# Kernel optimization log

Measured on AMD Instinct MI355X. Metric: run time of the kernel, lower is better.

The kernel has to match this reference:

```python
import jax, jax.numpy as jnp
import numpy as np
import math

VOCAB, D, H, NL, L, B = 50257, 768, 12, 4, 1024, 2
DH = D // H
DFF = 4 * D
ALPHA = 0.25
NEG = -1e9


def _ln(x, g, b, eps=1e-5):
    mu = x.mean(-1, keepdims=True)
    var = ((x - mu) ** 2).mean(-1, keepdims=True)
    return (x - mu) * jax.lax.rsqrt(var + eps) * g + b


def setup_inputs() -> dict:
    key = jax.random.key(0)
    ks = jax.random.split(key, 16)
    s = 0.02
    tokens = jax.random.randint(ks[0], (B, L), 0, VOCAB)
    timelike_mask = jax.random.randint(ks[1], (NL, D), 0, 2).astype(jnp.int32)
    embed = jax.random.normal(ks[2], (VOCAB, D), jnp.float32) * s
    pos_emb = jax.random.normal(ks[3], (L, D), jnp.float32) * s
    wq = jax.random.normal(ks[4], (NL, D, D), jnp.float32) * s
    wk = jax.random.normal(ks[5], (NL, D, D), jnp.float32) * s
    wv = jax.random.normal(ks[6], (NL, D, D), jnp.float32) * s
    wo = jax.random.normal(ks[7], (NL, D, D), jnp.float32) * s
    ff_w1 = jax.random.normal(ks[8], (NL, DFF, D), jnp.float32) * s
    ff_b1 = jnp.zeros((NL, DFF), jnp.float32)
    ff_w2 = jax.random.normal(ks[9], (NL, D, DFF), jnp.float32) * s
    ff_b2 = jnp.zeros((NL, D), jnp.float32)
    ln1_g = jnp.ones((NL, D), jnp.float32); ln1_b = jnp.zeros((NL, D), jnp.float32)
    ln2_g = jnp.ones((NL, D), jnp.float32); ln2_b = jnp.zeros((NL, D), jnp.float32)
    lnf_g = jnp.ones((D,), jnp.float32); lnf_b = jnp.zeros((D,), jnp.float32)
    return dict(tokens=tokens, timelike_mask=timelike_mask, embed=embed, pos_emb=pos_emb,
                wq=wq, wk=wk, wv=wv, wo=wo,
                ln1_g=ln1_g, ln1_b=ln1_b, ln2_g=ln2_g, ln2_b=ln2_b,
                ff_w1=ff_w1, ff_b1=ff_b1, ff_w2=ff_w2, ff_b2=ff_b2,
                lnf_g=lnf_g, lnf_b=lnf_b)


def reference(tokens, timelike_mask, embed, pos_emb, wq, wk, wv, wo,
              ln1_g, ln1_b, ln2_g, ln2_b, ff_w1, ff_b1, ff_w2, ff_b2,
              lnf_g, lnf_b):
    Bc, Lc = tokens.shape
    scale = math.sqrt(DH)
    # embeddings: token + learned position
    h = embed[tokens] + pos_emb[None, :Lc]  # (B,L,D)
    # additive causal mask, matching torch's -inf attention_mask convention
    causal = jnp.where(jnp.tril(jnp.ones((Lc, Lc), bool)), 0.0, NEG)[None, None]  # (1,1,L,L)
    for i in range(NL):
        xn = _ln(h, ln1_g[i], ln1_b[i])
        # nn.Linear(bias=False): y = x @ W.T, W is (out,in)
        q = jnp.einsum('bld,od->blo', xn, wq[i]).reshape(Bc, Lc, H, DH).astype(jnp.float32)
        k = jnp.einsum('bld,od->blo', xn, wk[i]).reshape(Bc, Lc, H, DH).astype(jnp.float32)
        v = jnp.einsum('bld,od->blo', xn, wv[i]).reshape(Bc, Lc, H, DH)
        # Minkowski term: scores_std - 2*alpha*(Q*P_t)K^T  ==  (Q*(1-2*alpha*m)) K^T
        m = timelike_mask[i].astype(jnp.float32).reshape(H, DH)  # per-head timelike directions
        q_eff = q * (1.0 - 2.0 * ALPHA * m)[None, None]
        scores = jnp.einsum('bqhd,bkhd->bhqk', q_eff, k) / scale + causal
        aw = jax.nn.softmax(scores, axis=-1)  # dropout=0 (eval)
        attn = jnp.einsum('bhqk,bkhd->bqhd', aw, v).reshape(Bc, Lc, D)
        h = h + jnp.einsum('bld,od->blo', attn, wo[i])
        xn2 = _ln(h, ln2_g[i], ln2_b[i])
        ff = jax.nn.gelu(jnp.einsum('bld,fd->blf', xn2, ff_w1[i]) + ff_b1[i], approximate=False)
        h = h + jnp.einsum('blf,df->bld', ff, ff_w2[i]) + ff_b2[i]
    h = _ln(h, lnf_g, lnf_b)
    logits = jnp.einsum('bld,vd->blv', h, embed)  # tied LM head
    return logits
```

## Files before the change

kernel.cpp:

```cpp
#include <hip/hip_runtime.h>
#include <math.h>

#define VOCABSZ 50257
#define VPAD 50304
#define DMODEL 768
#define NHEAD 12
#define NLAYER 4
#define SEQ 1024
#define BATCH 2
#define DHEAD 64
#define DFFN 3072
#define BT (BATCH * SEQ)
#define NBH (BATCH * NHEAD)

typedef __attribute__((ext_vector_type(8))) short bf16x8;
typedef __attribute__((ext_vector_type(4))) float f32x4;

__device__ __forceinline__ ushort f2bf(float f) {
  uint u = __builtin_bit_cast(uint, f);
  u = (u + 0x7fffu + ((u >> 16) & 1u)) >> 16;
  return (ushort)u;
}

__device__ __forceinline__ void gl_lds16(const ushort* g, ushort* l) {
  __builtin_amdgcn_global_load_lds(
      (const __attribute__((address_space(1))) void*)g,
      (__attribute__((address_space(3))) void*)l, 16, 0, 0);
}

__global__ __launch_bounds__(256) void conv4_kernel(
    const float* __restrict__ src, ushort* __restrict__ dst, int n4) {
  int i = blockIdx.x * 256 + threadIdx.x;
  if (i >= n4) return;
  float4 v = reinterpret_cast<const float4*>(src)[i];
  reinterpret_cast<ushort4*>(dst)[i] =
      make_ushort4(f2bf(v.x), f2bf(v.y), f2bf(v.z), f2bf(v.w));
}

__global__ __launch_bounds__(256) void conv_qkv_kernel(
    const float* __restrict__ src, ushort* __restrict__ dst, int qoff4) {
  const int per4 = DMODEL * DMODEL / 4;
  int i = blockIdx.x * 256 + threadIdx.x;
  if (i >= NLAYER * per4) return;
  int layer = i / per4, rem = i % per4;
  float4 v = reinterpret_cast<const float4*>(src)[i];
  reinterpret_cast<ushort4*>(dst)[(size_t)layer * (3 * per4) + qoff4 + rem] =
      make_ushort4(f2bf(v.x), f2bf(v.y), f2bf(v.z), f2bf(v.w));
}

__global__ __launch_bounds__(256) void conv_embed_kernel(
    const float* __restrict__ emb, ushort* __restrict__ dst) {
  int i = blockIdx.x * 256 + threadIdx.x;
  if (i >= VPAD * DMODEL / 4) return;
  int row = (i * 4) / DMODEL;
  ushort4 o = make_ushort4(0, 0, 0, 0);
  if (row < VOCABSZ) {
    float4 v = reinterpret_cast<const float4*>(emb)[i];
    o = make_ushort4(f2bf(v.x), f2bf(v.y), f2bf(v.z), f2bf(v.w));
  }
  reinterpret_cast<ushort4*>(dst)[i] = o;
}

__global__ __launch_bounds__(256) void embed_kernel(
    const int* __restrict__ tok, const float* __restrict__ emb,
    const float* __restrict__ pos, float* __restrict__ h) {
  int row = blockIdx.x;
  int l = row % SEQ;
  int t = tok[row];
  int tid = threadIdx.x;
#pragma unroll
  for (int j = 0; j < 3; ++j) {
    int c = tid + j * 256;
    h[(size_t)row * DMODEL + c] =
        emb[(size_t)t * DMODEL + c] + pos[(size_t)l * DMODEL + c];
  }
}

template <int KS, bool RBIAS>
__global__ __launch_bounds__(256) void ln_kernel(
    float* __restrict__ h, const float* __restrict__ part,
    const float* __restrict__ rb, const float* __restrict__ g,
    const float* __restrict__ bta, ushort* __restrict__ o) {
  __shared__ float red[8];
  int row = blockIdx.x;
  int tid = threadIdx.x;
  float* xr = h + (size_t)row * DMODEL;
  float v[3];
  float s = 0.f, sq = 0.f;
#pragma unroll
  for (int j = 0; j < 3; ++j) {
    int c = tid + j * 256;
    float a = xr[c];
    if (RBIAS) a += rb[c];
    if (KS > 0) {
#pragma unroll
      for (int z = 0; z < KS; ++z)
        a += part[(size_t)z * BT * DMODEL + (size_t)row * DMODEL + c];
      xr[c] = a;
    }
    v[j] = a;
    s += a;
    sq += a * a;
  }
#pragma unroll
  for (int off = 1; off < 64; off <<= 1) {
    s += __shfl_xor(s, off);
    sq += __shfl_xor(sq, off);
  }
  int wid = tid >> 6;
  if ((tid & 63) == 0) { red[wid * 2] = s; red[wid * 2 + 1] = sq; }
  __syncthreads();
  float S = red[0] + red[2] + red[4] + red[6];
  float SQ = red[1] + red[3] + red[5] + red[7];
  float mu = S * (1.0f / DMODEL);
  float var = SQ * (1.0f / DMODEL) - mu * mu;
  float r = rsqrtf(var + 1e-5f);
  ushort* orow = o + (size_t)row * DMODEL;
#pragma unroll
  for (int j = 0; j < 3; ++j) {
    int c = tid + j * 256;
    orow[c] = f2bf((v[j] - mu) * r * g[c] + bta[c]);
  }
}

__global__ __launch_bounds__(256) void vtrans_kernel(
    const ushort* __restrict__ v, ushort* __restrict__ vt) {
  __shared__ ushort t[64][65];
  int z = blockIdx.y, b = z / NHEAD, hh = z % NHEAD;
  int key0 = blockIdx.x * 64;
  int tid = threadIdx.x;
#pragma unroll
  for (int p = 0; p < 16; ++p) {
    int idx = tid + p * 256;
    int kk = idx >> 6, d = idx & 63;
    t[kk][d] = v[((size_t)(b * SEQ + key0 + kk)) * DMODEL + hh * DHEAD + d];
  }
  __syncthreads();
#pragma unroll
  for (int p = 0; p < 16; ++p) {
    int idx = tid + p * 256;
    int d = idx >> 6, kk = idx & 63;
    vt[((size_t)(z * 64 + d)) * SEQ + key0 + kk] = t[kk][d];
  }
}

__global__ __launch_bounds__(256) void fattn_kernel(
    const ushort* __restrict__ q, const ushort* __restrict__ k,
    const ushort* __restrict__ vt, ushort* __restrict__ o) {
  __shared__ __align__(16) ushort Ks[64 * 64];
  __shared__ __align__(16) ushort Vs[64 * 64];
  __shared__ __align__(16) ushort Ps[4][16][80];
  const int z = blockIdx.y, b = z / NHEAD, hh = z % NHEAD;
  const int q0 = (gridDim.x - 1 - blockIdx.x) * 64;
  const int tid = threadIdx.x, w = tid >> 6, l = tid & 63;
  const int fr = l & 15, ks = l >> 4;
  const int qrow = q0 + w * 16 + fr;
  const ushort* qp = q + (size_t)(b * SEQ + qrow) * DMODEL + hh * DHEAD;
  const bf16x8 qf0 = *reinterpret_cast<const bf16x8*>(qp + ks * 8);
  const bf16x8 qf1 = *reinterpret_cast<const bf16x8*>(qp + 32 + ks * 8);

  const int srow = w * 16 + (l >> 3);
  const int sslot = l & 7;

  f32x4 acc_o[4] = {};
  float mrun = -1e30f, lrun = 0.f;

  for (int k0 = 0; k0 <= q0; k0 += 64) {
#pragma unroll
    for (int c = 0; c < 2; ++c) {
      int r = srow + c * 8;
      int g = sslot ^ (r & 7);
      gl_lds16(k + (size_t)(b * SEQ + k0 + r) * DMODEL + hh * DHEAD + g * 8,
               Ks + (w * 16 + c * 8) * 64);
      gl_lds16(vt + (size_t)(z * 64 + r) * SEQ + k0 + g * 8,
               Vs + (w * 16 + c * 8) * 64);
    }
    __syncthreads();
    f32x4 acc_s[4] = {};
#pragma unroll
    for (int kstep = 0; kstep < 2; ++kstep) {
      const bf16x8 qf = kstep ? qf1 : qf0;
#pragma unroll
      for (int kb = 0; kb < 4; ++kb) {
        int ra = kb * 16 + fr;
        bf16x8 af = *reinterpret_cast<const bf16x8*>(
            Ks + ra * 64 + (((kstep * 4 + ks) ^ (ra & 7)) * 8));
        acc_s[kb] =
            __builtin_amdgcn_mfma_f32_16x16x32_bf16(af, qf, acc_s[kb], 0, 0, 0);
      }
    }
    const bool diag = (k0 == q0);
    float pm = -1e30f;
    float sv[4][4];
#pragma unroll
    for (int kb = 0; kb < 4; ++kb)
#pragma unroll
      for (int r = 0; r < 4; ++r) {
        float s = acc_s[kb][r];
        if (diag && (k0 + kb * 16 + ks * 4 + r > qrow)) s = -1e30f;
        sv[kb][r] = s;
        pm = fmaxf(pm, s);
      }
    pm = fmaxf(pm, __shfl_xor(pm, 16));
    pm = fmaxf(pm, __shfl_xor(pm, 32));
    float mnew = fmaxf(mrun, pm);
    float scale = __expf(mrun - mnew);
    float psum = 0.f;
#pragma unroll
    for (int kb = 0; kb < 4; ++kb) {
      float p0 = __expf(sv[kb][0] - mnew);
      float p1 = __expf(sv[kb][1] - mnew);
      float p2 = __expf(sv[kb][2] - mnew);
      float p3 = __expf(sv[kb][3] - mnew);
      psum += (p0 + p1) + (p2 + p3);
      *reinterpret_cast<ushort4*>(&Ps[w][fr][kb * 16 + ks * 4]) =
          make_ushort4(f2bf(p0), f2bf(p1), f2bf(p2), f2bf(p3));
    }
    psum += __shfl_xor(psum, 16);
    psum += __shfl_xor(psum, 32);
    lrun = lrun * scale + psum;
    mrun = mnew;
#pragma unroll
    for (int db = 0; db < 4; ++db) acc_o[db] *= scale;
#pragma unroll
    for (int kstep = 0; kstep < 2; ++kstep) {
      bf16x8 pf =
          *reinterpret_cast<const bf16x8*>(&Ps[w][fr][kstep * 32 + ks * 8]);
#pragma unroll
      for (int db = 0; db < 4; ++db) {
        int rd = db * 16 + fr;
        bf16x8 vf = *reinterpret_cast<const bf16x8*>(
            Vs + rd * 64 + (((kstep * 4 + ks) ^ (rd & 7)) * 8));
        acc_o[db] =
            __builtin_amdgcn_mfma_f32_16x16x32_bf16(vf, pf, acc_o[db], 0, 0, 0);
      }
    }
    __syncthreads();
  }
  float rinv = 1.0f / lrun;
#pragma unroll
  for (int db = 0; db < 4; ++db) {
    ushort4 o4 =
        make_ushort4(f2bf(acc_o[db][0] * rinv), f2bf(acc_o[db][1] * rinv),
                     f2bf(acc_o[db][2] * rinv), f2bf(acc_o[db][3] * rinv));
    *reinterpret_cast<ushort4*>(o + (size_t)(b * SEQ + qrow) * DMODEL +
                                hh * DHEAD + db * 16 + ks * 4) = o4;
  }
}

template <bool QKV, bool BIAS, bool GELU, bool RES, bool OUTBF, bool SWZ,
          bool PART>
__global__ __launch_bounds__(256) void gemm_bf16_nt(
    const ushort* __restrict__ A, const ushort* __restrict__ B,
    const float* __restrict__ bias, const int* __restrict__ tmask,
    const float* __restrict__ res, float* __restrict__ Cf,
    ushort* __restrict__ Cb, int ldc, ushort* __restrict__ qb,
    ushort* __restrict__ kb, ushort* __restrict__ vb, int M, int K, int Nreal,
    int kchunk) {
  __shared__ __align__(16) ushort As[2][128 * 32];
  __shared__ __align__(16) ushort Bs[2][128 * 32];
  int bnx, bmy;
  if (SWZ) {
    int bid = blockIdx.x;
    int chunk = gridDim.x >> 3;
    int wgid = (bid & 7) * chunk + (bid >> 3);
    int mb = M >> 7;
    bmy = wgid % mb;
    bnx = wgid / mb;
  } else {
    bnx = blockIdx.x;
    bmy = blockIdx.y;
  }
  const int m0 = bmy * 128, n0 = bnx * 128;
  const int kbeg = PART ? blockIdx.z * kchunk : 0;
  const int kend = PART ? kbeg + kchunk : K;
  if (PART) Cf += (size_t)blockIdx.z * M * ldc;
  const int tid = threadIdx.x;
  const int w = tid >> 6, l = tid & 63;
  const int wr = w >> 1, wc = w & 1;
  const int fr = l & 15, ks = l >> 4;

  const int seg0 = w * 2, seg1 = w * 2 + 1;
  const int srow0 = seg0 * 16 + (l >> 2);
  const int srow1 = seg1 * 16 + (l >> 2);
  const int koff0 = (((l & 3) ^ ((srow0 >> 1) & 3))) * 8;
  const int koff1 = (((l & 3) ^ ((srow1 >> 1) & 3))) * 8;
  const ushort* A0 = A + (size_t)(m0 + srow0) * K + koff0;
  const ushort* A1 = A + (size_t)(m0 + srow1) * K + koff1;
  const ushort* B0 = B + (size_t)(n0 + srow0) * K + koff0;
  const ushort* B1 = B + (size_t)(n0 + srow1) * K + koff1;

  int aoff[4], boff[4];
#pragma unroll
  for (int i = 0; i < 4; ++i) {
    int ra = wr * 64 + i * 16 + fr;
    aoff[i] = ra * 32 + ((ks ^ ((ra >> 1) & 3)) * 8);
    int rb = wc * 64 + i * 16 + fr;
    boff[i] = rb * 32 + ((ks ^ ((rb >> 1) & 3)) * 8);
  }

  gl_lds16(A0 + kbeg, &As[0][seg0 * 512]);
  gl_lds16(A1 + kbeg, &As[0][seg1 * 512]);
  gl_lds16(B0 + kbeg, &Bs[0][seg0 * 512]);
  gl_lds16(B1 + kbeg, &Bs[0][seg1 * 512]);
  __syncthreads();

  f32x4 acc[4][4] = {};
  int cur = 0;
  for (int k0 = kbeg; k0 < kend; k0 += 32) {
    const int nxt = k0 + 32;
    if (nxt < kend) {
      gl_lds16(A0 + nxt, &As[cur ^ 1][seg0 * 512]);
      gl_lds16(A1 + nxt, &As[cur ^ 1][seg1 * 512]);
      gl_lds16(B0 + nxt, &Bs[cur ^ 1][seg0 * 512]);
      gl_lds16(B1 + nxt, &Bs[cur ^ 1][seg1 * 512]);
    }
    bf16x8 af[4], bfr[4];
#pragma unroll
    for (int i = 0; i < 4; ++i)
      af[i] = *reinterpret_cast<const bf16x8*>(&As[cur][aoff[i]]);
#pragma unroll
    for (int i = 0; i < 4; ++i)
      bfr[i] = *reinterpret_cast<const bf16x8*>(&Bs[cur][boff[i]]);
#pragma unroll
    for (int mi = 0; mi < 4; ++mi)
#pragma unroll
      for (int nj = 0; nj < 4; ++nj)
        acc[mi][nj] = __builtin_amdgcn_mfma_f32_16x16x32_bf16(
            af[mi], bfr[nj], acc[mi][nj], 0, 0, 0);
    __syncthreads();
    cur ^= 1;
  }

#pragma unroll
  for (int mi = 0; mi < 4; ++mi) {
#pragma unroll
    for (int nj = 0; nj < 4; ++nj) {
      int n = n0 + wc * 64 + nj * 16 + fr;
      if (n < Nreal) {
#pragma unroll
        for (int r = 0; r < 4; ++r) {
          int m = m0 + wr * 64 + mi * 16 + ks * 4 + r;
          float v = acc[mi][nj][r];
          if (PART) {
            Cf[(size_t)m * ldc + n] = v;
          } else if (QKV) {
            if (n < DMODEL) {
              v *= (1.0f - 0.5f * (float)tmask[n]) * 0.125f;
              qb[(size_t)m * DMODEL + n] = f2bf(v);
            } else if (n < 2 * DMODEL) {
              kb[(size_t)m * DMODEL + (n - DMODEL)] = f2bf(v);
            } else {
              vb[(size_t)m * DMODEL + (n - 2 * DMODEL)] = f2bf(v);
            }
          } else {
            if (BIAS) v += bias[n];
            if (GELU) v = 0.5f * v * (1.0f + erff(v * 0.70710678118f));
            if (RES) v += res[(size_t)m * ldc + n];
            if (OUTBF)
              Cb[(size_t)m * ldc + n] = f2bf(v);
            else
              Cf[(size_t)m * ldc + n] = v;
          }
        }
      }
    }
  }
}

extern "C" void kernel_launch(void* const* d_in, const int* in_sizes, int n_in,
                              void* d_out, int out_size, void* d_ws,
                              size_t ws_size, hipStream_t stream) {
  const int* tokens = (const int*)d_in[0];
  const int* tmask = (const int*)d_in[1];
  const float* embed = (const float*)d_in[2];
  const float* pos = (const float*)d_in[3];
  const float* wq = (const float*)d_in[4];
  const float* wk = (const float*)d_in[5];
  const float* wv = (const float*)d_in[6];
  const float* wo = (const float*)d_in[7];
  const float* ln1g = (const float*)d_in[8];
  const float* ln1b = (const float*)d_in[9];
  const float* ln2g = (const float*)d_in[10];
  const float* ln2b = (const float*)d_in[11];
  const float* fw1 = (const float*)d_in[12];
  const float* fb1 = (const float*)d_in[13];
  const float* fw2 = (const float*)d_in[14];
  const float* fb2 = (const float*)d_in[15];
  const float* lnfg = (const float*)d_in[16];
  const float* lnfb = (const float*)d_in[17];

  char* wp = (char*)d_ws;
  auto alloc = [&](size_t bytes) {
    void* p = wp;
    wp += (bytes + 255) & ~(size_t)255;
    return p;
  };
  float* h = (float*)alloc((size_t)BT * DMODEL * 4);
  float* part = (float*)alloc((size_t)4 * BT * DMODEL * 4);
  ushort* qb = (ushort*)alloc((size_t)BT * DMODEL * 2);
  ushort* kb = (ushort*)alloc((size_t)BT * DMODEL * 2);
  ushort* vb = (ushort*)alloc((size_t)BT * DMODEL * 2);
  ushort* vt = (ushort*)alloc((size_t)NBH * DHEAD * SEQ * 2);
  ushort* xn = (ushort*)alloc((size_t)BT * DMODEL * 2);
  ushort* ab = (ushort*)alloc((size_t)BT * DMODEL * 2);
  ushort* ffb = (ushort*)alloc((size_t)BT * DFFN * 2);
  ushort* wqkv_b = (ushort*)alloc((size_t)NLAYER * 3 * DMODEL * DMODEL * 2);
  ushort* wo_b = (ushort*)alloc((size_t)NLAYER * DMODEL * DMODEL * 2);
  ushort* fw1_b = (ushort*)alloc((size_t)NLAYER * DFFN * DMODEL * 2);
  ushort* fw2_b = (ushort*)alloc((size_t)NLAYER * DMODEL * DFFN * 2);
  ushort* emb_b = (ushort*)alloc((size_t)VPAD * DMODEL * 2);

  const int per4 = DMODEL * DMODEL / 4;
  conv_qkv_kernel<<<(NLAYER * per4 + 255) / 256, 256, 0, stream>>>(wq, wqkv_b, 0);
  conv_qkv_kernel<<<(NLAYER * per4 + 255) / 256, 256, 0, stream>>>(wk, wqkv_b, per4);
  conv_qkv_kernel<<<(NLAYER * per4 + 255) / 256, 256, 0, stream>>>(wv, wqkv_b, 2 * per4);
  conv4_kernel<<<(NLAYER * per4 + 255) / 256, 256, 0, stream>>>(wo, wo_b, NLAYER * per4);
  const int nff4 = NLAYER * DFFN * DMODEL / 4;
  conv4_kernel<<<(nff4 + 255) / 256, 256, 0, stream>>>(fw1, fw1_b, nff4);
  conv4_kernel<<<(nff4 + 255) / 256, 256, 0, stream>>>(fw2, fw2_b, nff4);
  conv_embed_kernel<<<(VPAD * DMODEL / 4 + 255) / 256, 256, 0, stream>>>(embed, emb_b);

  embed_kernel<<<BT, 256, 0, stream>>>(tokens, embed, pos, h);

  const dim3 gqkv(3 * DMODEL / 128, BT / 128);
  const dim3 gff(DFFN / 128, BT / 128);
  const dim3 gwo(DMODEL / 128, BT / 128, 2);
  const dim3 gff2(DMODEL / 128, BT / 128, 4);
  const dim3 gv((BT / 128) * (VPAD / 128));

  for (int i = 0; i < NLAYER; ++i) {
    if (i == 0)
      ln_kernel<0, false><<<BT, 256, 0, stream>>>(
          h, nullptr, nullptr, ln1g + i * DMODEL, ln1b + i * DMODEL, xn);
    else
      ln_kernel<4, true><<<BT, 256, 0, stream>>>(
          h, part, fb2 + (i - 1) * DMODEL, ln1g + i * DMODEL,
          ln1b + i * DMODEL, xn);

    gemm_bf16_nt<true, false, false, false, false, false, false>
        <<<gqkv, 256, 0, stream>>>(
            xn, wqkv_b + (size_t)i * 3 * DMODEL * DMODEL, nullptr,
            tmask + i * DMODEL, nullptr, nullptr, nullptr, 0, qb, kb, vb, BT,
            DMODEL, 3 * DMODEL, DMODEL);

    vtrans_kernel<<<dim3(SEQ / 64, NBH), 256, 0, stream>>>(vb, vt);

    fattn_kernel<<<dim3(SEQ / 64, NBH), 256, 0, stream>>>(qb, kb, vt, ab);

    gemm_bf16_nt<false, false, false, false, false, false, true>
        <<<gwo, 256, 0, stream>>>(
            ab, wo_b + (size_t)i * DMODEL * DMODEL, nullptr, nullptr, nullptr,
            part, nullptr, DMODEL, nullptr, nullptr, nullptr, BT, DMODEL,
            DMODEL, DMODEL / 2);

    ln_kernel<2, false><<<BT, 256, 0, stream>>>(
        h, part, nullptr, ln2g + i * DMODEL, ln2b + i * DMODEL, xn);

    gemm_bf16_nt<false, true, true, false, true, false, false>
        <<<gff, 256, 0, stream>>>(
            xn, fw1_b + (size_t)i * DFFN * DMODEL, fb1 + i * DFFN, nullptr,
            nullptr, nullptr, ffb, DFFN, nullptr, nullptr, nullptr, BT, DMODEL,
            DFFN, DMODEL);

    gemm_bf16_nt<false, false, false, false, false, false, true>
        <<<gff2, 256, 0, stream>>>(
            ffb, fw2_b + (size_t)i * DMODEL * DFFN, nullptr, nullptr, nullptr,
            part, nullptr, DMODEL, nullptr, nullptr, nullptr, BT, DFFN, DMODEL,
            DFFN / 4);
  }

  ln_kernel<4, true><<<BT, 256, 0, stream>>>(
      h, part, fb2 + (NLAYER - 1) * DMODEL, lnfg, lnfb, xn);

  gemm_bf16_nt<false, false, false, false, false, true, false>
      <<<gv, 256, 0, stream>>>(
          xn, emb_b, nullptr, nullptr, nullptr, (float*)d_out, nullptr,
          VOCABSZ, nullptr, nullptr, nullptr, BT, DMODEL, VOCABSZ, DMODEL);
}
```

Before: 973.1 us.

## Add 256x256 pipelined LM-head GEMM and fuse V transpose into QKV epilogue

Replaces the generic 128x128 LM-head GEMM with a dedicated 512-thread kernel using 256x256 tiles, a 4-stage LDS ring with three tiles prefetched, split MFMA phases with s_setprio, and an XCD-aware block swizzle. VPAD grows to a multiple of 256 so the tile grid covers it. The QKV GEMM epilogue now writes V directly in the transposed per-head layout, removing the separate vtrans kernel and the intermediate V buffer. Risks include higher register and LDS pressure in the new kernel, extra padded work, and strided ushort4 stores for the transposed V.

```diff
diff --git a/kernel.cpp b/kernel.cpp
--- a/kernel.cpp
+++ b/kernel.cpp
@@ -2,7 +2,7 @@
 #include <math.h>
 
 #define VOCABSZ 50257
-#define VPAD 50304
+#define VPAD 50432
 #define DMODEL 768
 #define NHEAD 12
 #define NLAYER 4
@@ -120,27 +120,6 @@
   for (int j = 0; j < 3; ++j) {
     int c = tid + j * 256;
     orow[c] = f2bf((v[j] - mu) * r * g[c] + bta[c]);
-  }
-}
-
-__global__ __launch_bounds__(256) void vtrans_kernel(
-    const ushort* __restrict__ v, ushort* __restrict__ vt) {
-  __shared__ ushort t[64][65];
-  int z = blockIdx.y, b = z / NHEAD, hh = z % NHEAD;
-  int key0 = blockIdx.x * 64;
-  int tid = threadIdx.x;
-#pragma unroll
-  for (int p = 0; p < 16; ++p) {
-    int idx = tid + p * 256;
-    int kk = idx >> 6, d = idx & 63;
-    t[kk][d] = v[((size_t)(b * SEQ + key0 + kk)) * DMODEL + hh * DHEAD + d];
-  }
-  __syncthreads();
-#pragma unroll
-  for (int p = 0; p < 16; ++p) {
-    int idx = tid + p * 256;
-    int d = idx >> 6, kk = idx & 63;
-    vt[((size_t)(z * 64 + d)) * SEQ + key0 + kk] = t[kk][d];
   }
 }
 
@@ -248,30 +227,17 @@
   }
 }
 
-template <bool QKV, bool BIAS, bool GELU, bool RES, bool OUTBF, bool SWZ,
-          bool PART>
+template <bool QKV, bool BIAS, bool GELU, bool RES, bool OUTBF, bool PART>
 __global__ __launch_bounds__(256) void gemm_bf16_nt(
     const ushort* __restrict__ A, const ushort* __restrict__ B,
     const float* __restrict__ bias, const int* __restrict__ tmask,
     const float* __restrict__ res, float* __restrict__ Cf,
     ushort* __restrict__ Cb, int ldc, ushort* __restrict__ qb,
-    ushort* __restrict__ kb, ushort* __restrict__ vb, int M, int K, int Nreal,
+    ushort* __restrict__ kb, ushort* __restrict__ vt, int M, int K, int Nreal,
     int kchunk) {
   __shared__ __align__(16) ushort As[2][128 * 32];
   __shared__ __align__(16) ushort Bs[2][128 * 32];
-  int bnx, bmy;
-  if (SWZ) {
-    int bid = blockIdx.x;
-    int chunk = gridDim.x >> 3;
-    int wgid = (bid & 7) * chunk + (bid >> 3);
-    int mb = M >> 7;
-    bmy = wgid % mb;
-    bnx = wgid / mb;
-  } else {
-    bnx = blockIdx.x;
-    bmy = blockIdx.y;
-  }
-  const int m0 = bmy * 128, n0 = bnx * 128;
+  const int m0 = blockIdx.y * 128, n0 = blockIdx.x * 128;
   const int kbeg = PART ? blockIdx.z * kchunk : 0;
   const int kend = PART ? kbeg + kchunk : K;
   if (PART) Cf += (size_t)blockIdx.z * M * ldc;
@@ -338,22 +304,40 @@
     for (int nj = 0; nj < 4; ++nj) {
       int n = n0 + wc * 64 + nj * 16 + fr;
       if (n < Nreal) {
-#pragma unroll
-        for (int r = 0; r < 4; ++r) {
-          int m = m0 + wr * 64 + mi * 16 + ks * 4 + r;
-          float v = acc[mi][nj][r];
-          if (PART) {
-            Cf[(size_t)m * ldc + n] = v;
-          } else if (QKV) {
-            if (n < DMODEL) {
-              v *= (1.0f - 0.5f * (float)tmask[n]) * 0.125f;
-              qb[(size_t)m * DMODEL + n] = f2bf(v);
-            } else if (n < 2 * DMODEL) {
-              kb[(size_t)m * DMODEL + (n - DMODEL)] = f2bf(v);
-            } else {
-              vb[(size_t)m * DMODEL + (n - 2 * DMODEL)] = f2bf(v);
+        if (PART) {
+#pragma unroll
+          for (int r = 0; r < 4; ++r) {
+            int m = m0 + wr * 64 + mi * 16 + ks * 4 + r;
+            Cf[(size_t)m * ldc + n] = acc[mi][nj][r];
+          }
+        } else if (QKV) {
+          if (n < DMODEL) {
+            float sc = (1.0f - 0.5f * (float)tmask[n]) * 0.125f;
+#pragma unroll
+            for (int r = 0; r < 4; ++r) {
+              int m = m0 + wr * 64 + mi * 16 + ks * 4 + r;
+              qb[(size_t)m * DMODEL + n] = f2bf(acc[mi][nj][r] * sc);
+            }
+          } else if (n < 2 * DMODEL) {
+#pragma unroll
+            for (int r = 0; r < 4; ++r) {
+              int m = m0 + wr * 64 + mi * 16 + ks * 4 + r;
+              kb[(size_t)m * DMODEL + (n - DMODEL)] = f2bf(acc[mi][nj][r]);
             }
           } else {
+            int d = n - 2 * DMODEL;
+            int key = (m0 & (SEQ - 1)) + wr * 64 + mi * 16 + ks * 4;
+            size_t zr = (size_t)((m0 >> 10) * NHEAD + (d >> 6)) * 64 + (d & 63);
+            ushort4 p4 = make_ushort4(
+                f2bf(acc[mi][nj][0]), f2bf(acc[mi][nj][1]),
+                f2bf(acc[mi][nj][2]), f2bf(acc[mi][nj][3]));
+            *reinterpret_cast<ushort4*>(vt + zr * SEQ + key) = p4;
+          }
+        } else {
+#pragma unroll
+          for (int r = 0; r < 4; ++r) {
+            int m = m0 + wr * 64 + mi * 16 + ks * 4 + r;
+            float v = acc[mi][nj][r];
             if (BIAS) v += bias[n];
             if (GELU) v = 0.5f * v * (1.0f + erff(v * 0.70710678118f));
             if (RES) v += res[(size_t)m * ldc + n];
@@ -363,6 +347,112 @@
               Cf[(size_t)m * ldc + n] = v;
           }
         }
+      }
+    }
+  }
+}
+
+__global__ __launch_bounds__(512, 2) void gemm_lmhead(
+    const ushort* __restrict__ A, const ushort* __restrict__ B,
+    float* __restrict__ C) {
+  __shared__ __align__(16) ushort As[4][256 * 32];
+  __shared__ __align__(16) ushort Bs[4][256 * 32];
+  const int K = DMODEL;
+  const int NT = K / 32;
+
+  const int bid = blockIdx.x;
+  const int chunk = gridDim.x >> 3;
+  const int wgid = (bid & 7) * chunk + (bid >> 3);
+  const int m0 = (wgid & 7) * 256;
+  const int n0 = (wgid >> 3) * 256;
+
+  const int tid = threadIdx.x;
+  const int w = tid >> 6, l = tid & 63;
+  const int wr = w >> 2, wc = w & 3;
+  const int fr = l & 15, ks = l >> 4;
+
+  const int g8 = ((l & 3) ^ ((l >> 3) & 3)) * 8;
+  const int sr = w * 16 + (l >> 2);
+  const int aswz = (ks ^ ((fr >> 1) & 3)) * 8;
+  int aoff[8], boff[4];
+#pragma unroll
+  for (int mi = 0; mi < 8; ++mi)
+    aoff[mi] = (wr * 128 + mi * 16 + fr) * 32 + aswz;
+#pragma unroll
+  for (int nj = 0; nj < 4; ++nj)
+    boff[nj] = (wc * 64 + nj * 16 + fr) * 32 + aswz;
+
+  auto stA = [&](int t, int c) {
+    gl_lds16(A + (size_t)(m0 + c * 128 + sr) * K + t * 32 + g8,
+             &As[t & 3][(c * 128 + w * 16) * 32]);
+  };
+  auto stB = [&](int t, int c) {
+    gl_lds16(B + (size_t)(n0 + c * 128 + sr) * K + t * 32 + g8,
+             &Bs[t & 3][(c * 128 + w * 16) * 32]);
+  };
+
+#pragma unroll
+  for (int pt = 0; pt < 3; ++pt) {
+    stA(pt, 0); stA(pt, 1); stB(pt, 0); stB(pt, 1);
+  }
+  asm volatile("s_waitcnt vmcnt(8)" ::: "memory");
+  __builtin_amdgcn_s_barrier();
+
+  f32x4 acc[8][4] = {};
+  for (int t = 0; t < NT; ++t) {
+    const ushort* Asl = &As[t & 3][0];
+    const ushort* Bsl = &Bs[t & 3][0];
+    const bool pf = (t + 3 < NT);
+    bf16x8 bfr[4], af[4];
+#pragma unroll
+    for (int nj = 0; nj < 4; ++nj)
+      bfr[nj] = *reinterpret_cast<const bf16x8*>(Bsl + boff[nj]);
+#pragma unroll
+    for (int mi = 0; mi < 4; ++mi)
+      af[mi] = *reinterpret_cast<const bf16x8*>(Asl + aoff[mi]);
+    if (pf) { stA(t + 3, 0); stA(t + 3, 1); }
+    __builtin_amdgcn_s_barrier();
+    __builtin_amdgcn_s_setprio(1);
+#pragma unroll
+    for (int mi = 0; mi < 4; ++mi)
+#pragma unroll
+      for (int nj = 0; nj < 4; ++nj)
+        acc[mi][nj] = __builtin_amdgcn_mfma_f32_16x16x32_bf16(
+            af[mi], bfr[nj], acc[mi][nj], 0, 0, 0);
+    __builtin_amdgcn_s_setprio(0);
+    __builtin_amdgcn_s_barrier();
+#pragma unroll
+    for (int mi = 0; mi < 4; ++mi)
+      af[mi] = *reinterpret_cast<const bf16x8*>(Asl + aoff[mi + 4]);
+    if (pf) { stB(t + 3, 0); stB(t + 3, 1); }
+    __builtin_amdgcn_s_barrier();
+    __builtin_amdgcn_s_setprio(1);
+#pragma unroll
+    for (int mi = 0; mi < 4; ++mi)
+#pragma unroll
+      for (int nj = 0; nj < 4; ++nj)
+        acc[mi + 4][nj] = __builtin_amdgcn_mfma_f32_16x16x32_bf16(
+            af[mi], bfr[nj], acc[mi + 4][nj], 0, 0, 0);
+    __builtin_amdgcn_s_setprio(0);
+    if (t + 3 < NT)
+      asm volatile("s_waitcnt vmcnt(8)" ::: "memory");
+    else if (t + 2 < NT)
+      asm volatile("s_waitcnt vmcnt(4)" ::: "memory");
+    else
+      asm volatile("s_waitcnt vmcnt(0)" ::: "memory");
+    __builtin_amdgcn_s_barrier();
+  }
+
+#pragma unroll
+  for (int mi = 0; mi < 8; ++mi) {
+#pragma unroll
+    for (int nj = 0; nj < 4; ++nj) {
+      int n = n0 + wc * 64 + nj * 16 + fr;
+      if (n < VOCABSZ) {
+        int m = m0 + wr * 128 + mi * 16 + ks * 4;
+#pragma unroll
+        for (int r = 0; r < 4; ++r)
+          C[(size_t)(m + r) * VOCABSZ + n] = acc[mi][nj][r];
       }
     }
   }
@@ -400,7 +490,6 @@
   float* part = (float*)alloc((size_t)4 * BT * DMODEL * 4);
   ushort* qb = (ushort*)alloc((size_t)BT * DMODEL * 2);
   ushort* kb = (ushort*)alloc((size_t)BT * DMODEL * 2);
-  ushort* vb = (ushort*)alloc((size_t)BT * DMODEL * 2);
   ushort* vt = (ushort*)alloc((size_t)NBH * DHEAD * SEQ * 2);
   ushort* xn = (ushort*)alloc((size_t)BT * DMODEL * 2);
   ushort* ab = (ushort*)alloc((size_t)BT * DMODEL * 2);
@@ -427,7 +516,6 @@
   const dim3 gff(DFFN / 128, BT / 128);
   const dim3 gwo(DMODEL / 128, BT / 128, 2);
   const dim3 gff2(DMODEL / 128, BT / 128, 4);
-  const dim3 gv((BT / 128) * (VPAD / 128));
 
   for (int i = 0; i < NLAYER; ++i) {
     if (i == 0)
@@ -438,17 +526,15 @@
           h, part, fb2 + (i - 1) * DMODEL, ln1g + i * DMODEL,
           ln1b + i * DMODEL, xn);
 
-    gemm_bf16_nt<true, false, false, false, false, false, false>
+    gemm_bf16_nt<true, false, false, false, false, false>
         <<<gqkv, 256, 0, stream>>>(
             xn, wqkv_b + (size_t)i * 3 * DMODEL * DMODEL, nullptr,
-            tmask + i * DMODEL, nullptr, nullptr, nullptr, 0, qb, kb, vb, BT,
+            tmask + i * DMODEL, nullptr, nullptr, nullptr, 0, qb, kb, vt, BT,
             DMODEL, 3 * DMODEL, DMODEL);
 
-    vtrans_kernel<<<dim3(SEQ / 64, NBH), 256, 0, stream>>>(vb, vt);
-
     fattn_kernel<<<dim3(SEQ / 64, NBH), 256, 0, stream>>>(qb, kb, vt, ab);
 
-    gemm_bf16_nt<false, false, false, false, false, false, true>
+    gemm_bf16_nt<false, false, false, false, false, true>
         <<<gwo, 256, 0, stream>>>(
             ab, wo_b + (size_t)i * DMODEL * DMODEL, nullptr, nullptr, nullptr,
             part, nullptr, DMODEL, nullptr, nullptr, nullptr, BT, DMODEL,
@@ -457,13 +543,13 @@
     ln_kernel<2, false><<<BT, 256, 0, stream>>>(
         h, part, nullptr, ln2g + i * DMODEL, ln2b + i * DMODEL, xn);
 
-    gemm_bf16_nt<false, true, true, false, true, false, false>
+    gemm_bf16_nt<false, true, true, false, true, false>
         <<<gff, 256, 0, stream>>>(
             xn, fw1_b + (size_t)i * DFFN * DMODEL, fb1 + i * DFFN, nullptr,
             nullptr, nullptr, ffb, DFFN, nullptr, nullptr, nullptr, BT, DMODEL,
             DFFN, DMODEL);
 
-    gemm_bf16_nt<false, false, false, false, false, false, true>
+    gemm_bf16_nt<false, false, false, false, false, true>
         <<<gff2, 256, 0, stream>>>(
             ffb, fw2_b + (size_t)i * DMODEL * DFFN, nullptr, nullptr, nullptr,
             part, nullptr, DMODEL, nullptr, nullptr, nullptr, BT, DFFN, DMODEL,
@@ -473,8 +559,5 @@
   ln_kernel<4, true><<<BT, 256, 0, stream>>>(
       h, part, fb2 + (NLAYER - 1) * DMODEL, lnfg, lnfb, xn);
 
-  gemm_bf16_nt<false, false, false, false, false, true, false>
-      <<<gv, 256, 0, stream>>>(
-          xn, emb_b, nullptr, nullptr, nullptr, (float*)d_out, nullptr,
-          VOCABSZ, nullptr, nullptr, nullptr, BT, DMODEL, VOCABSZ, DMODEL);
-}
+  gemm_lmhead<<<8 * (VPAD / 256), 512, 0, stream>>>(xn, emb_b, (float*)d_out);
+}
```

New measurement: 941.7 us. 1.03x faster.

## Fuse V transpose into QKV GEMM epilogue and relax GEMM barriers

Applied to the files above, without the earlier changes.

The QKV GEMM epilogue now writes V directly in the transposed per-head layout (vectorized 4-element stores along the key dimension), so the separate vtrans kernel and its intermediate buffer go away. The GEMM main loop replaces __syncthreads with explicit vmcnt waits plus raw s_barrier and sched_barrier, letting the next tile's loads stay in flight while the current tile is consumed. VPAD is raised to 50432, which changes the LM-head grid size and the padded embedding buffer. The manual waitcnt logic relies on the gl_lds16 load count and could cause ordering hazards if that assumption is wrong.

```diff
diff --git a/kernel.cpp b/kernel.cpp
--- a/kernel.cpp
+++ b/kernel.cpp
@@ -2,7 +2,7 @@
 #include <math.h>
 
 #define VOCABSZ 50257
-#define VPAD 50304
+#define VPAD 50432
 #define DMODEL 768
 #define NHEAD 12
 #define NLAYER 4
@@ -120,27 +120,6 @@
   for (int j = 0; j < 3; ++j) {
     int c = tid + j * 256;
     orow[c] = f2bf((v[j] - mu) * r * g[c] + bta[c]);
-  }
-}
-
-__global__ __launch_bounds__(256) void vtrans_kernel(
-    const ushort* __restrict__ v, ushort* __restrict__ vt) {
-  __shared__ ushort t[64][65];
-  int z = blockIdx.y, b = z / NHEAD, hh = z % NHEAD;
-  int key0 = blockIdx.x * 64;
-  int tid = threadIdx.x;
-#pragma unroll
-  for (int p = 0; p < 16; ++p) {
-    int idx = tid + p * 256;
-    int kk = idx >> 6, d = idx & 63;
-    t[kk][d] = v[((size_t)(b * SEQ + key0 + kk)) * DMODEL + hh * DHEAD + d];
-  }
-  __syncthreads();
-#pragma unroll
-  for (int p = 0; p < 16; ++p) {
-    int idx = tid + p * 256;
-    int d = idx >> 6, kk = idx & 63;
-    vt[((size_t)(z * 64 + d)) * SEQ + key0 + kk] = t[kk][d];
   }
 }
 
@@ -255,7 +234,7 @@
     const float* __restrict__ bias, const int* __restrict__ tmask,
     const float* __restrict__ res, float* __restrict__ Cf,
     ushort* __restrict__ Cb, int ldc, ushort* __restrict__ qb,
-    ushort* __restrict__ kb, ushort* __restrict__ vb, int M, int K, int Nreal,
+    ushort* __restrict__ kb, ushort* __restrict__ vt, int M, int K, int Nreal,
     int kchunk) {
   __shared__ __align__(16) ushort As[2][128 * 32];
   __shared__ __align__(16) ushort Bs[2][128 * 32];
@@ -303,7 +282,6 @@
   gl_lds16(A1 + kbeg, &As[0][seg1 * 512]);
   gl_lds16(B0 + kbeg, &Bs[0][seg0 * 512]);
   gl_lds16(B1 + kbeg, &Bs[0][seg1 * 512]);
-  __syncthreads();
 
   f32x4 acc[4][4] = {};
   int cur = 0;
@@ -314,7 +292,12 @@
       gl_lds16(A1 + nxt, &As[cur ^ 1][seg1 * 512]);
       gl_lds16(B0 + nxt, &Bs[cur ^ 1][seg0 * 512]);
       gl_lds16(B1 + nxt, &Bs[cur ^ 1][seg1 * 512]);
-    }
+      asm volatile("s_waitcnt vmcnt(4)" ::: "memory");
+    } else {
+      asm volatile("s_waitcnt vmcnt(0)" ::: "memory");
+    }
+    __builtin_amdgcn_s_barrier();
+    __builtin_amdgcn_sched_barrier(0);
     bf16x8 af[4], bfr[4];
 #pragma unroll
     for (int i = 0; i < 4; ++i)
@@ -328,7 +311,8 @@
       for (int nj = 0; nj < 4; ++nj)
         acc[mi][nj] = __builtin_amdgcn_mfma_f32_16x16x32_bf16(
             af[mi], bfr[nj], acc[mi][nj], 0, 0, 0);
-    __syncthreads();
+    __builtin_amdgcn_sched_barrier(0);
+    __builtin_amdgcn_s_barrier();
     cur ^= 1;
   }
 
@@ -338,22 +322,40 @@
     for (int nj = 0; nj < 4; ++nj) {
       int n = n0 + wc * 64 + nj * 16 + fr;
       if (n < Nreal) {
-#pragma unroll
-        for (int r = 0; r < 4; ++r) {
-          int m = m0 + wr * 64 + mi * 16 + ks * 4 + r;
-          float v = acc[mi][nj][r];
-          if (PART) {
-            Cf[(size_t)m * ldc + n] = v;
-          } else if (QKV) {
-            if (n < DMODEL) {
-              v *= (1.0f - 0.5f * (float)tmask[n]) * 0.125f;
-              qb[(size_t)m * DMODEL + n] = f2bf(v);
-            } else if (n < 2 * DMODEL) {
-              kb[(size_t)m * DMODEL + (n - DMODEL)] = f2bf(v);
-            } else {
-              vb[(size_t)m * DMODEL + (n - 2 * DMODEL)] = f2bf(v);
+        if (PART) {
+#pragma unroll
+          for (int r = 0; r < 4; ++r) {
+            int m = m0 + wr * 64 + mi * 16 + ks * 4 + r;
+            Cf[(size_t)m * ldc + n] = acc[mi][nj][r];
+          }
+        } else if (QKV) {
+          if (n < DMODEL) {
+            float sc = (1.0f - 0.5f * (float)tmask[n]) * 0.125f;
+#pragma unroll
+            for (int r = 0; r < 4; ++r) {
+              int m = m0 + wr * 64 + mi * 16 + ks * 4 + r;
+              qb[(size_t)m * DMODEL + n] = f2bf(acc[mi][nj][r] * sc);
+            }
+          } else if (n < 2 * DMODEL) {
+#pragma unroll
+            for (int r = 0; r < 4; ++r) {
+              int m = m0 + wr * 64 + mi * 16 + ks * 4 + r;
+              kb[(size_t)m * DMODEL + (n - DMODEL)] = f2bf(acc[mi][nj][r]);
             }
           } else {
+            int d = n - 2 * DMODEL;
+            int key = (m0 & (SEQ - 1)) + wr * 64 + mi * 16 + ks * 4;
+            size_t zr = (size_t)((m0 >> 10) * NHEAD + (d >> 6)) * 64 + (d & 63);
+            ushort4 p4 = make_ushort4(
+                f2bf(acc[mi][nj][0]), f2bf(acc[mi][nj][1]),
+                f2bf(acc[mi][nj][2]), f2bf(acc[mi][nj][3]));
+            *reinterpret_cast<ushort4*>(vt + zr * SEQ + key) = p4;
+          }
+        } else {
+#pragma unroll
+          for (int r = 0; r < 4; ++r) {
+            int m = m0 + wr * 64 + mi * 16 + ks * 4 + r;
+            float v = acc[mi][nj][r];
             if (BIAS) v += bias[n];
             if (GELU) v = 0.5f * v * (1.0f + erff(v * 0.70710678118f));
             if (RES) v += res[(size_t)m * ldc + n];
@@ -400,7 +402,6 @@
   float* part = (float*)alloc((size_t)4 * BT * DMODEL * 4);
   ushort* qb = (ushort*)alloc((size_t)BT * DMODEL * 2);
   ushort* kb = (ushort*)alloc((size_t)BT * DMODEL * 2);
-  ushort* vb = (ushort*)alloc((size_t)BT * DMODEL * 2);
   ushort* vt = (ushort*)alloc((size_t)NBH * DHEAD * SEQ * 2);
   ushort* xn = (ushort*)alloc((size_t)BT * DMODEL * 2);
   ushort* ab = (ushort*)alloc((size_t)BT * DMODEL * 2);
@@ -427,7 +428,7 @@
   const dim3 gff(DFFN / 128, BT / 128);
   const dim3 gwo(DMODEL / 128, BT / 128, 2);
   const dim3 gff2(DMODEL / 128, BT / 128, 4);
-  const dim3 gv((BT / 128) * (VPAD / 128));
+  const int gv = (BT / 128) * (VPAD / 128);
 
   for (int i = 0; i < NLAYER; ++i) {
     if (i == 0)
@@ -441,10 +442,8 @@
     gemm_bf16_nt<true, false, false, false, false, false, false>
         <<<gqkv, 256, 0, stream>>>(
             xn, wqkv_b + (size_t)i * 3 * DMODEL * DMODEL, nullptr,
-            tmask + i * DMODEL, nullptr, nullptr, nullptr, 0, qb, kb, vb, BT,
+            tmask + i * DMODEL, nullptr, nullptr, nullptr, 0, qb, kb, vt, BT,
             DMODEL, 3 * DMODEL, DMODEL);
-
-    vtrans_kernel<<<dim3(SEQ / 64, NBH), 256, 0, stream>>>(vb, vt);
 
     fattn_kernel<<<dim3(SEQ / 64, NBH), 256, 0, stream>>>(qb, kb, vt, ab);
 
```

After: 927.2 us. -4.7%, faster.
